# Optimization experiments

Hardware: AMD Instinct MI355X
Metric: run time of the kernel (lower is better)

## Reference

```python
import jax, jax.numpy as jnp
import numpy as np

NOISE_STD = 0.1

def setup_inputs() -> dict:
    key = jax.random.key(0)
    k1, k2, k3, k4 = jax.random.split(key, 4)
    B, S, D, E, NS = 4, 4096, 2048, 64, 10
    x = jax.random.normal(k1, (B, S, D), dtype=jnp.float32)
    W = jax.random.normal(k2, (E, D), dtype=jnp.float32) * (1.0 / np.sqrt(D))
    scale_condition = jax.random.normal(k3, (NS, 1, 1), dtype=jnp.float32)
    noise = jax.random.normal(k4, (B, S, E), dtype=jnp.float32)
    return {"x": x, "W": W, "scale_condition": scale_condition, "noise": noise, "scale_idx": 3}

def reference(x, W, scale_condition, noise, scale_idx):
    TOP_K = 2
    E = W.shape[0]
    # scale modulation: scale_condition[scale_idx] has shape [1,1], broadcasts over [B,S,D]
    scale_factor = scale_condition[scale_idx]
    router_input = x * (1.0 + scale_factor * 0.1)
    # small GEMM: [B,S,D] x [D,E] -> [B,S,E]
    router_logits = jnp.einsum('bsd,ed->bse', router_input, W)
    router_logits = router_logits + noise * NOISE_STD
    routing_probs = jax.nn.softmax(router_logits, axis=-1)
    routing_weights, selected_experts = jax.lax.top_k(routing_probs, TOP_K)
    routing_weights = routing_weights / jnp.sum(routing_weights, axis=-1, keepdims=True)
    # scatter top-k normalized weights into dense [B,S,E] dispatch tensor
    dispatch_tensor = jnp.sum(
        jax.nn.one_hot(selected_experts, E, dtype=routing_weights.dtype)
        * routing_weights[..., None],
        axis=-2,
    )
    return dispatch_tensor, routing_probs, selected_experts
```

## Files before the change

kernel.cpp:

```cpp
#include <hip/hip_runtime.h>
#include <math.h>

#define D        2048
#define E        64
#define NROWS    16384

#define ROWS_PB  32
#define BKC      64
#define NCH      (D / BKC)
#define LDX      72
#define LDW      72
#define XSH      (ROWS_PB * LDX)
#define WSH      (E * LDW)
#define BUF_SHORTS (2 * XSH + 2 * WSH)

#define LSCALE   2048.0f
#define S1       4.8828125e-4f
#define S2       2.384185791015625e-7f

typedef __attribute__((ext_vector_type(8))) _Float16 f16x8;
typedef __attribute__((ext_vector_type(4))) float f32x4;

__device__ unsigned short g_whi[(size_t)E * D];
__device__ unsigned short g_wlo[(size_t)E * D];

__device__ __forceinline__ unsigned short f2h(float f) {
    union { _Float16 h; unsigned short u; } c;
    c.h = (_Float16)f;
    return c.u;
}
__device__ __forceinline__ float h2f(unsigned short u) {
    union { _Float16 h; unsigned short u; } c;
    c.u = u;
    return (float)c.h;
}

__global__ __launch_bounds__(256)
void w_cvt(const float* __restrict__ W)
{
    const int i = (blockIdx.x * 256 + threadIdx.x) << 3;
    const float4 a = *(const float4*)(W + i);
    const float4 b = *(const float4*)(W + i + 4);
    float vv[8] = {a.x, a.y, a.z, a.w, b.x, b.y, b.z, b.w};
    unsigned int hw[4], lw[4];
#pragma unroll
    for (int j = 0; j < 4; ++j) {
        const unsigned short h0 = f2h(vv[2*j]);
        const unsigned short h1 = f2h(vv[2*j+1]);
        const unsigned short l0 = f2h((vv[2*j]   - h2f(h0)) * LSCALE);
        const unsigned short l1 = f2h((vv[2*j+1] - h2f(h1)) * LSCALE);
        hw[j] = (unsigned int)h0 | ((unsigned int)h1 << 16);
        lw[j] = (unsigned int)l0 | ((unsigned int)l1 << 16);
    }
    *(uint4*)(g_whi + i) = make_uint4(hw[0], hw[1], hw[2], hw[3]);
    *(uint4*)(g_wlo + i) = make_uint4(lw[0], lw[1], lw[2], lw[3]);
}

__global__ __launch_bounds__(512, 4)
void moe_fused(const float* __restrict__ x,
               const float* __restrict__ scond,
               const int* __restrict__ sidx,
               const float* __restrict__ noise,
               float* __restrict__ dispatch,
               float* __restrict__ probs,
               float* __restrict__ sel)
{
    __shared__ unsigned short smem[2 * BUF_SHORTS];

    const int t = threadIdx.x;
    const int l = t & 63;
    const int w = t >> 6;

    const float factor = 1.0f + 0.1f * scond[sidx[0]];

    const int xr_ = t >> 4;
    const int xc_ = (t & 15) << 2;
    const int we_ = t >> 3;
    const int wk_ = (t & 7) << 3;

    const int R  = (w >> 2) << 4;
    const int CB = (w & 3) << 4;
    const int fr = l & 15;
    const int fq = l >> 4;

    const int rowG0 = blockIdx.x * ROWS_PB;

    const float* xg = x + (size_t)(rowG0 + xr_) * D + xc_;
    const unsigned short* wgh = g_whi + (size_t)we_ * D + wk_;
    const unsigned short* wgl = g_wlo + (size_t)we_ * D + wk_;

    f32x4 acch = {0.f,0.f,0.f,0.f};
    f32x4 accm = {0.f,0.f,0.f,0.f};
    f32x4 accl = {0.f,0.f,0.f,0.f};

    float4 xp  = *(const float4*)(xg);
    uint4  wph = *(const uint4*)(wgh);
    uint4  wpl = *(const uint4*)(wgl);

    for (int c = 0; c < NCH; ++c) {
        unsigned short* base = smem + (c & 1) * BUF_SHORTS;
        unsigned short* xh = base;
        unsigned short* xl = base + XSH;
        unsigned short* wh = base + 2 * XSH;
        unsigned short* wl = wh + WSH;

        {
            const float v0 = xp.x * factor, v1 = xp.y * factor;
            const float v2 = xp.z * factor, v3 = xp.w * factor;
            const unsigned short h0 = f2h(v0), h1 = f2h(v1);
            const unsigned short h2 = f2h(v2), h3 = f2h(v3);
            const unsigned short q0 = f2h((v0 - h2f(h0)) * LSCALE);
            const unsigned short q1 = f2h((v1 - h2f(h1)) * LSCALE);
            const unsigned short q2 = f2h((v2 - h2f(h2)) * LSCALE);
            const unsigned short q3 = f2h((v3 - h2f(h3)) * LSCALE);
            uint2 hw, lw;
            hw.x = (unsigned int)h0 | ((unsigned int)h1 << 16);
            hw.y = (unsigned int)h2 | ((unsigned int)h3 << 16);
            lw.x = (unsigned int)q0 | ((unsigned int)q1 << 16);
            lw.y = (unsigned int)q2 | ((unsigned int)q3 << 16);
            const int o = xr_ * LDX + xc_;
            *(uint2*)&xh[o] = hw;
            *(uint2*)&xl[o] = lw;
        }
        {
            const int o = we_ * LDW + wk_;
            *(uint4*)&wh[o] = wph;
            *(uint4*)&wl[o] = wpl;
        }

        __syncthreads();

        if (c + 1 < NCH) {
            const int kn = (c + 1) * BKC;
            xp  = *(const float4*)(xg + kn);
            wph = *(const uint4*)(wgh + kn);
            wpl = *(const uint4*)(wgl + kn);
        }

#pragma unroll
        for (int ks = 0; ks < 2; ++ks) {
            const int ko = (ks << 5) + (fq << 3);
            const f16x8 ah = *(const f16x8*)&xh[(R + fr) * LDX + ko];
            const f16x8 al = *(const f16x8*)&xl[(R + fr) * LDX + ko];
            const f16x8 bh = *(const f16x8*)&wh[(CB + fr) * LDW + ko];
            const f16x8 bl = *(const f16x8*)&wl[(CB + fr) * LDW + ko];
            acch = __builtin_amdgcn_mfma_f32_16x16x32_f16(ah, bh, acch, 0, 0, 0);
            accm = __builtin_amdgcn_mfma_f32_16x16x32_f16(ah, bl, accm, 0, 0, 0);
            accm = __builtin_amdgcn_mfma_f32_16x16x32_f16(al, bh, accm, 0, 0, 0);
            accl = __builtin_amdgcn_mfma_f32_16x16x32_f16(al, bl, accl, 0, 0, 0);
        }
    }

    __syncthreads();
    float* lg = (float*)smem;
#pragma unroll
    for (int j = 0; j < 4; ++j) {
        const int rr = R + (fq << 2) + j;
        lg[rr * 68 + CB + fr] = acch[j] + S1 * accm[j] + S2 * accl[j];
    }
    __syncthreads();

    const int r0 = w << 2;
#pragma unroll
    for (int i = 0; i < 4; ++i) {
        const int G = rowG0 + r0 + i;
        const float v = lg[(r0 + i) * 68 + l] + 0.1f * noise[(size_t)G * E + l];

        float m = v;
#pragma unroll
        for (int off = 32; off > 0; off >>= 1)
            m = fmaxf(m, __shfl_xor(m, off, 64));
        const float p = expf(v - m);
        float s = p;
#pragma unroll
        for (int off = 32; off > 0; off >>= 1)
            s += __shfl_xor(s, off, 64);
        const float prob = p / s;
        probs[(size_t)G * E + l] = prob;

        float bv = prob; int bi = l;
#pragma unroll
        for (int off = 32; off > 0; off >>= 1) {
            const float ov = __shfl_xor(bv, off, 64);
            const int   oi = __shfl_xor(bi, off, 64);
            if (ov > bv || (ov == bv && oi < bi)) { bv = ov; bi = oi; }
        }
        float cv = (l == bi) ? -INFINITY : prob;
        int ci = l;
#pragma unroll
        for (int off = 32; off > 0; off >>= 1) {
            const float ov = __shfl_xor(cv, off, 64);
            const int   oi = __shfl_xor(ci, off, 64);
            if (ov > cv || (ov == cv && oi < ci)) { cv = ov; ci = oi; }
        }

        const float sum2 = bv + cv;
        float dval = 0.f;
        if (l == bi) dval = bv / sum2;
        if (l == ci) dval = cv / sum2;
        dispatch[(size_t)G * E + l] = dval;

        if (l == 0) {
            float2 sv; sv.x = (float)bi; sv.y = (float)ci;
            *(float2*)(sel + (size_t)G * 2) = sv;
        }
    }
}

extern "C" void kernel_launch(void* const* d_in, const int* in_sizes, int n_in,
                              void* d_out, int out_size, void* d_ws, size_t ws_size,
                              hipStream_t stream) {
    const float* x     = (const float*)d_in[0];
    const float* W     = (const float*)d_in[1];
    const float* scond = (const float*)d_in[2];
    const float* noise = (const float*)d_in[3];
    const int*   sidx  = (const int*)d_in[4];

    float* out      = (float*)d_out;
    float* dispatch = out;
    float* probs    = out + (size_t)NROWS * E;
    float* sel      = out + 2 * (size_t)NROWS * E;

    (void)d_ws; (void)ws_size;

    w_cvt<<<dim3(64), dim3(256), 0, stream>>>(W);
    moe_fused<<<dim3(NROWS / ROWS_PB), dim3(512), 0, stream>>>(
        x, scond, sidx, noise, dispatch, probs, sel);
}
```

Baseline: 228.0 us.

## Stage x and W tiles into LDS via async global_load_lds with XOR swizzle

Replaces the register-staged prefetch with direct global-to-LDS DMA loads (global_load_lds, 16 bytes per lane) into double-buffered shared memory with an XOR-swizzled layout instead of padding. x is now kept as fp32 in LDS, and each wave does the hi/lo fp16 split at fragment-read time instead of once at store time. The aim is to overlap the next chunk's global loads with MFMA work and free registers for the loads. The cost is that the split is repeated by each wave that reads the same x rows, and x takes twice as many LDS bytes.

```diff
diff --git a/kernel.cpp b/kernel.cpp
--- a/kernel.cpp
+++ b/kernel.cpp
@@ -8,11 +8,10 @@
 #define ROWS_PB  32
 #define BKC      64
 #define NCH      (D / BKC)
-#define LDX      72
-#define LDW      72
-#define XSH      (ROWS_PB * LDX)
-#define WSH      (E * LDW)
-#define BUF_SHORTS (2 * XSH + 2 * WSH)
+#define XOFF     0
+#define WHOFF    8192
+#define WLOFF    16384
+#define BUFB     24576
 
 #define LSCALE   2048.0f
 #define S1       4.8828125e-4f
@@ -21,8 +20,8 @@
 typedef __attribute__((ext_vector_type(8))) _Float16 f16x8;
 typedef __attribute__((ext_vector_type(4))) float f32x4;
 
-__device__ unsigned short g_whi[(size_t)E * D];
-__device__ unsigned short g_wlo[(size_t)E * D];
+__device__ __attribute__((aligned(16))) unsigned short g_whi[(size_t)E * D];
+__device__ __attribute__((aligned(16))) unsigned short g_wlo[(size_t)E * D];
 
 __device__ __forceinline__ unsigned short f2h(float f) {
     union { _Float16 h; unsigned short u; } c;
@@ -33,6 +32,32 @@
     union { _Float16 h; unsigned short u; } c;
     c.u = u;
     return (float)c.h;
+}
+
+__device__ __forceinline__ void dma16(const void* g, void* l) {
+    __builtin_amdgcn_global_load_lds(
+        (const __attribute__((address_space(1))) unsigned int*)g,
+        (__attribute__((address_space(3))) unsigned int*)l,
+        16, 0, 0);
+}
+
+__device__ __forceinline__ void split8(float4 A, float4 B, float f,
+                                       f16x8& hi, f16x8& lo) {
+    float v[8] = {A.x * f, A.y * f, A.z * f, A.w * f,
+                  B.x * f, B.y * f, B.z * f, B.w * f};
+    unsigned int hw[4], lw[4];
+#pragma unroll
+    for (int j = 0; j < 4; ++j) {
+        const unsigned short h0 = f2h(v[2*j]);
+        const unsigned short h1 = f2h(v[2*j+1]);
+        const unsigned short l0 = f2h((v[2*j]   - h2f(h0)) * LSCALE);
+        const unsigned short l1 = f2h((v[2*j+1] - h2f(h1)) * LSCALE);
+        hw[j] = (unsigned int)h0 | ((unsigned int)h1 << 16);
+        lw[j] = (unsigned int)l0 | ((unsigned int)l1 << 16);
+    }
+    union { uint4 u; f16x8 h; } ch, cl;
+    ch.u = make_uint4(hw[0], hw[1], hw[2], hw[3]); hi = ch.h;
+    cl.u = make_uint4(lw[0], lw[1], lw[2], lw[3]); lo = cl.h;
 }
 
 __global__ __launch_bounds__(256)
@@ -65,94 +90,77 @@
                float* __restrict__ probs,
                float* __restrict__ sel)
 {
-    __shared__ unsigned short smem[2 * BUF_SHORTS];
+    __shared__ float4 smem_q[2 * BUFB / 16];
+    unsigned char* const sm = (unsigned char*)smem_q;
 
     const int t = threadIdx.x;
     const int l = t & 63;
     const int w = t >> 6;
 
     const float factor = 1.0f + 0.1f * scond[sidx[0]];
-
-    const int xr_ = t >> 4;
-    const int xc_ = (t & 15) << 2;
-    const int we_ = t >> 3;
-    const int wk_ = (t & 7) << 3;
 
     const int R  = (w >> 2) << 4;
     const int CB = (w & 3) << 4;
     const int fr = l & 15;
     const int fq = l >> 4;
+    const int sw = fr & 7;
 
     const int rowG0 = blockIdx.x * ROWS_PB;
 
-    const float* xg = x + (size_t)(rowG0 + xr_) * D + xc_;
-    const unsigned short* wgh = g_whi + (size_t)we_ * D + wk_;
-    const unsigned short* wgl = g_wlo + (size_t)we_ * D + wk_;
+    const float* xsrc =
+        x + (size_t)(rowG0 + (t >> 4)) * D + (((t & 15) ^ ((t >> 4) & 7)) << 2);
+    const unsigned short* whsrc =
+        g_whi + (size_t)(t >> 3) * D + (((t & 7) ^ ((t >> 3) & 7)) << 3);
+    const unsigned short* wlsrc =
+        g_wlo + (size_t)(t >> 3) * D + (((t & 7) ^ ((t >> 3) & 7)) << 3);
+
+    const int wb = w << 10;
 
     f32x4 acch = {0.f,0.f,0.f,0.f};
     f32x4 accm = {0.f,0.f,0.f,0.f};
     f32x4 accl = {0.f,0.f,0.f,0.f};
 
-    float4 xp  = *(const float4*)(xg);
-    uint4  wph = *(const uint4*)(wgh);
-    uint4  wpl = *(const uint4*)(wgl);
+#define STAGE(B, CC) do { \
+    unsigned char* const bb_ = sm + (B) * BUFB; \
+    dma16(xsrc  + (size_t)(CC) * BKC, bb_ + XOFF  + wb); \
+    dma16(whsrc + (size_t)(CC) * BKC, bb_ + WHOFF + wb); \
+    dma16(wlsrc + (size_t)(CC) * BKC, bb_ + WLOFF + wb); \
+} while (0)
+
+    STAGE(0, 0);
+    asm volatile("s_waitcnt vmcnt(0)" ::: "memory");
+    __syncthreads();
 
     for (int c = 0; c < NCH; ++c) {
-        unsigned short* base = smem + (c & 1) * BUF_SHORTS;
-        unsigned short* xh = base;
-        unsigned short* xl = base + XSH;
-        unsigned short* wh = base + 2 * XSH;
-        unsigned short* wl = wh + WSH;
-
-        {
-            const float v0 = xp.x * factor, v1 = xp.y * factor;
-            const float v2 = xp.z * factor, v3 = xp.w * factor;
-            const unsigned short h0 = f2h(v0), h1 = f2h(v1);
-            const unsigned short h2 = f2h(v2), h3 = f2h(v3);
-            const unsigned short q0 = f2h((v0 - h2f(h0)) * LSCALE);
-            const unsigned short q1 = f2h((v1 - h2f(h1)) * LSCALE);
-            const unsigned short q2 = f2h((v2 - h2f(h2)) * LSCALE);
-            const unsigned short q3 = f2h((v3 - h2f(h3)) * LSCALE);
-            uint2 hw, lw;
-            hw.x = (unsigned int)h0 | ((unsigned int)h1 << 16);
-            hw.y = (unsigned int)h2 | ((unsigned int)h3 << 16);
-            lw.x = (unsigned int)q0 | ((unsigned int)q1 << 16);
-            lw.y = (unsigned int)q2 | ((unsigned int)q3 << 16);
-            const int o = xr_ * LDX + xc_;
-            *(uint2*)&xh[o] = hw;
-            *(uint2*)&xl[o] = lw;
-        }
-        {
-            const int o = we_ * LDW + wk_;
-            *(uint4*)&wh[o] = wph;
-            *(uint4*)&wl[o] = wpl;
-        }
-
-        __syncthreads();
-
-        if (c + 1 < NCH) {
-            const int kn = (c + 1) * BKC;
-            xp  = *(const float4*)(xg + kn);
-            wph = *(const uint4*)(wgh + kn);
-            wpl = *(const uint4*)(wgl + kn);
-        }
+        const int cur = c & 1;
+        if (c + 1 < NCH) STAGE(cur ^ 1, c + 1);
+
+        const unsigned char* bb = sm + cur * BUFB;
+        const float* xb = (const float*)(bb + XOFF);
+        const unsigned short* whb = (const unsigned short*)(bb + WHOFF);
+        const unsigned short* wlb = (const unsigned short*)(bb + WLOFF);
 
 #pragma unroll
         for (int ks = 0; ks < 2; ++ks) {
-            const int ko = (ks << 5) + (fq << 3);
-            const f16x8 ah = *(const f16x8*)&xh[(R + fr) * LDX + ko];
-            const f16x8 al = *(const f16x8*)&xl[(R + fr) * LDX + ko];
-            const f16x8 bh = *(const f16x8*)&wh[(CB + fr) * LDW + ko];
-            const f16x8 bl = *(const f16x8*)&wl[(CB + fr) * LDW + ko];
+            const int ls0 = (ks << 3) + (fq << 1);
+            const float4 xa = *(const float4*)(xb + ((R + fr) << 6) + ((ls0 ^ sw) << 2));
+            const float4 xv = *(const float4*)(xb + ((R + fr) << 6) + (((ls0 + 1) ^ sw) << 2));
+            f16x8 ah, al;
+            split8(xa, xv, factor, ah, al);
+            const int lw_ = (ks << 2) + fq;
+            const f16x8 bh = *(const f16x8*)(whb + ((CB + fr) << 6) + ((lw_ ^ sw) << 3));
+            const f16x8 bl = *(const f16x8*)(wlb + ((CB + fr) << 6) + ((lw_ ^ sw) << 3));
             acch = __builtin_amdgcn_mfma_f32_16x16x32_f16(ah, bh, acch, 0, 0, 0);
             accm = __builtin_amdgcn_mfma_f32_16x16x32_f16(ah, bl, accm, 0, 0, 0);
             accm = __builtin_amdgcn_mfma_f32_16x16x32_f16(al, bh, accm, 0, 0, 0);
             accl = __builtin_amdgcn_mfma_f32_16x16x32_f16(al, bl, accl, 0, 0, 0);
         }
-    }
-
-    __syncthreads();
-    float* lg = (float*)smem;
+
+        __syncthreads();
+    }
+#undef STAGE
+
+    float* lg = (float*)sm;
 #pragma unroll
     for (int j = 0; j < 4; ++j) {
         const int rr = R + (fq << 2) + j;
```

New measurement: 224.5 us. Within noise of the previous version (-1.6%).
